# Kernel optimization log

Measured on AMD Instinct MI355X. Metric: run time of the kernel, lower is better.

The kernel has to match this reference:

```python
import jax, jax.numpy as jnp
import numpy as np

N = 100_000      # nodes
E = 1_600_000    # edges
F_IN = 128       # node_features
H1, H2 = 50, 20  # GCLSTM hidden sizes (fixed in the model)


def _norm_weights(src, dst, w, n):
    # PyG get_laplacian(sym): remove self loops, deg over row, sym-normalize.
    w = jnp.where(src == dst, jnp.zeros_like(w), w)  # remove self-loops (weight 0)
    deg = jax.ops.segment_sum(w, src, num_segments=n)
    deg_safe = jnp.where(deg > 0, deg, jnp.ones_like(deg))
    dis = jnp.where(deg > 0, deg_safe ** -0.5, jnp.zeros_like(deg))
    return dis[src] * w * dis[dst]


def _lhat_matvec(x, src, dst, wn, n):
    # L_hat = 2*L/lambda_max - I with sym norm and lambda_max=2  =>  -D^-1/2 A D^-1/2
    return -jax.ops.segment_sum(wn[:, None] * x[src], dst, num_segments=n)


def _gclstm_cell(x, src, dst, wn, n, Wx, bx, theta, bconv, out_ch):
    # One GCLSTM step with H = C = 0 (the model passes H=C=None).
    H = jnp.zeros((n, out_ch), x.dtype)
    C = jnp.zeros((n, out_ch), x.dtype)
    # ChebConv(H) for all 4 gates: Tx_0 = H, Tx_1 = L_hat @ H   (K = 2)
    Tx = jnp.stack([H, _lhat_matvec(H, src, dst, wn, n)])       # [2, n, out]
    conv = jnp.einsum('knf,gkfo->gno', Tx, theta) + bconv[:, None, :]  # [4, n, out]
    Z = x @ Wx + bx                                              # [n, 4*out], gates i,f,c,o
    zi, zf, zc, zo = jnp.split(Z, 4, axis=-1)
    I = jax.nn.sigmoid(zi + conv[0])
    Fg = jax.nn.sigmoid(zf + conv[1])
    T = jnp.tanh(zc + conv[2])
    C = Fg * C + I * T
    O = jax.nn.sigmoid(zo + conv[3])
    return O * jnp.tanh(C)


def setup_inputs() -> dict:
    key = jax.random.key(0)
    ks = jax.random.split(key, 14)
    s = 0.1  # param init scale
    return {
        'x': jax.random.normal(ks[0], (N, F_IN), jnp.float32),
        'edge_index': jax.random.randint(ks[1], (2, E), 0, N, dtype=jnp.int32),
        'edge_weight': jax.random.uniform(ks[2], (E,), jnp.float32),
        # layer 1: W_x for gates i,f,c,o concatenated, Cheb thetas [gate, K, in, out]
        'Wx1': s * jax.random.normal(ks[3], (F_IN, 4 * H1), jnp.float32),
        'bx1': s * jax.random.normal(ks[4], (4 * H1,), jnp.float32),
        'theta1': s * jax.random.normal(ks[5], (4, 2, H1, H1), jnp.float32),
        'bconv1': s * jax.random.normal(ks[6], (4, H1), jnp.float32),
        # layer 2
        'Wx2': s * jax.random.normal(ks[7], (H1, 4 * H2), jnp.float32),
        'bx2': s * jax.random.normal(ks[8], (4 * H2,), jnp.float32),
        'theta2': s * jax.random.normal(ks[9], (4, 2, H2, H2), jnp.float32),
        'bconv2': s * jax.random.normal(ks[10], (4, H2), jnp.float32),
        # linear head
        'Wl': s * jax.random.normal(ks[11], (H2, 1), jnp.float32),
        'bl': s * jax.random.normal(ks[12], (1,), jnp.float32),
    }


def reference(x, edge_index, edge_weight, Wx1, bx1, theta1, bconv1,
              Wx2, bx2, theta2, bconv2, Wl, bl):
    src, dst = edge_index[0], edge_index[1]
    wn = _norm_weights(src, dst, edge_weight, N)
    h = _gclstm_cell(x, src, dst, wn, N, Wx1, bx1, theta1, bconv1, H1)
    h = _gclstm_cell(h, src, dst, wn, N, Wx2, bx2, theta2, bconv2, H2)
    h = jax.nn.relu(h)
    # F.dropout: identity at inference (deterministic baseline)
    return h @ Wl + bl  # [N, 1]
```

## Files before the change

kernel.cpp:

```cpp
#include <hip/hip_runtime.h>


#define NODES 100000
#define NTILES 6250

typedef float v4f   __attribute__((ext_vector_type(4)));
typedef float fragC __attribute__((ext_vector_type(4)));
typedef short frag8 __attribute__((ext_vector_type(8)));

#define OFF_B1H 0
#define OFF_B2H 40960
#define OFF_B2L 49152
#define OFF_BIAS1 57344
#define OFF_BIAS2 57984
#define OFF_WL 58240
#define OFF_BL 58320

__device__ __forceinline__ unsigned short f2bf(float f) {
  unsigned int u = __float_as_uint(f);
  u += 0x7fffu + ((u >> 16) & 1u);
  return (unsigned short)(u >> 16);
}
__device__ __forceinline__ float bf2f(unsigned short h) {
  return __uint_as_float(((unsigned int)h) << 16);
}
__device__ __forceinline__ float fsig(float z) {
  float t = __builtin_amdgcn_exp2f(z * -1.44269504088896f);
  return __builtin_amdgcn_rcpf(1.0f + t);
}
__device__ __forceinline__ float ftanh(float z) {
  float t = __builtin_amdgcn_exp2f(z * 2.88539008177793f);
  return 1.0f - 2.0f * __builtin_amdgcn_rcpf(t + 1.0f);
}

__device__ __forceinline__ void cvt8(const float* v, frag8& hi, frag8& lo) {
#pragma unroll
  for (int j = 0; j < 8; ++j) {
    unsigned short hs = f2bf(v[j]);
    float fh = bf2f(hs);
    hi[j] = (short)hs;
    lo[j] = (short)f2bf(v[j] - fh);
  }
}

__global__ void pack_weights(const float* __restrict__ Wx1, const float* __restrict__ bx1,
                             const float* __restrict__ bconv1,
                             const float* __restrict__ Wx2, const float* __restrict__ bx2,
                             const float* __restrict__ bconv2,
                             const float* __restrict__ Wl, const float* __restrict__ bl,
                             unsigned char* __restrict__ ws) {
  const int tid = blockIdx.x * blockDim.x + threadIdx.x;
  const int stride = gridDim.x * blockDim.x;
  unsigned short* B1H = (unsigned short*)(ws + OFF_B1H);
  unsigned short* B2H = (unsigned short*)(ws + OFF_B2H);
  unsigned short* B2L = (unsigned short*)(ws + OFF_B2L);
  float* BIAS1 = (float*)(ws + OFF_BIAS1);
  float* BIAS2 = (float*)(ws + OFF_BIAS2);
  float* WLp = (float*)(ws + OFF_WL);
  float* BLp = (float*)(ws + OFF_BL);

  for (int idx = tid; idx < 20480; idx += stride) {
    int j = idx & 7, lane = (idx >> 3) & 63, ft = idx >> 9;
    int s = ft / 10, t = ft % 10;
    int k = 32 * s + ((lane >> 4) << 3) + j;
    int n = 16 * t + (lane & 15);
    float val = 0.f;
    if (n < 150) {
      int g = n / 50, ch = n % 50;
      int gs = (g == 0) ? 0 : (g == 1) ? 2 : 3;
      val = Wx1[k * 200 + gs * 50 + ch];
    }
    B1H[idx] = f2bf(val);
  }
  for (int idx = tid; idx < 4096; idx += stride) {
    int j = idx & 7, lane = (idx >> 3) & 63, ft = idx >> 9;
    int s = ft >> 2, t = ft & 3;
    int k = 32 * s + ((lane >> 4) << 3) + j;
    int n = 16 * t + (lane & 15);
    float val = 0.f;
    if (k < 50 && n < 60) {
      int g = n / 20, ch = n % 20;
      int gs = (g == 0) ? 0 : (g == 1) ? 2 : 3;
      val = Wx2[k * 80 + gs * 20 + ch];
    }
    unsigned short h = f2bf(val);
    B2H[idx] = h;
    B2L[idx] = f2bf(val - bf2f(h));
  }
  for (int idx = tid; idx < 160; idx += stride) {
    float v = 0.f;
    if (idx < 150) {
      int g = idx / 50, ch = idx % 50;
      int gs = (g == 0) ? 0 : (g == 1) ? 2 : 3;
      v = bx1[gs * 50 + ch] + bconv1[gs * 50 + ch];
    }
    BIAS1[idx] = v;
  }
  for (int idx = tid; idx < 64; idx += stride) {
    float v = 0.f;
    if (idx < 60) {
      int g = idx / 20, ch = idx % 20;
      int gs = (g == 0) ? 0 : (g == 1) ? 2 : 3;
      v = bx2[gs * 20 + ch] + bconv2[gs * 20 + ch];
    }
    BIAS2[idx] = v;
  }
  for (int idx = tid; idx < 20; idx += stride) WLp[idx] = Wl[idx];
  if (tid == 0) BLp[0] = bl[0];
}

__global__ __launch_bounds__(256, 1) void gclstm_main(
    const float* __restrict__ x, const unsigned char* __restrict__ wsb,
    float* __restrict__ out) {
  __shared__ float sZ[4][16 * 161];
  __shared__ float sH[4][16 * 76];
  __shared__ float sBias1[160];
  __shared__ float sBias2[64];
  __shared__ float sWl[20];

  const int tid = threadIdx.x;
  const int lane = tid & 63;
  const int wave = tid >> 6;
  const int m = lane & 15;
  const int q = lane >> 4;

  if (tid < 160) sBias1[tid] = ((const float*)(wsb + OFF_BIAS1))[tid];
  if (tid < 64) sBias2[tid] = ((const float*)(wsb + OFF_BIAS2))[tid];
  if (tid < 20) sWl[tid] = ((const float*)(wsb + OFF_WL))[tid];
  for (int i = tid; i < 4 * 16 * 76; i += 256) ((float*)sH)[i] = 0.f;
  const float blv = *(const float*)(wsb + OFF_BL);
  __syncthreads();

  frag8 b1h[40], b2h[8], b2l[8];
  {
    const frag8* g1 = (const frag8*)(wsb + OFF_B1H);
#pragma unroll
    for (int i = 0; i < 40; ++i) b1h[i] = g1[i * 64 + lane];
    const frag8* g2h = (const frag8*)(wsb + OFF_B2H);
    const frag8* g2l = (const frag8*)(wsb + OFF_B2L);
#pragma unroll
    for (int i = 0; i < 8; ++i) {
      b2h[i] = g2h[i * 64 + lane];
      b2l[i] = g2l[i * 64 + lane];
    }
  }

  float* sZw = (float*)sZ + wave * (16 * 161);
  float* sHw = (float*)sH + wave * (16 * 76);
  const int gw = blockIdx.x * 4 + wave;

  v4f abuf[8];
  int tau = gw;
  {
    const float* xr = x + (size_t)(tau * 16 + m) * 128 + q * 8;
#pragma unroll
    for (int s = 0; s < 4; ++s) {
      abuf[2 * s] = *(const v4f*)(xr + 32 * s);
      abuf[2 * s + 1] = *(const v4f*)(xr + 32 * s + 4);
    }
  }

  for (; tau < NTILES; tau += 1024) {
    frag8 ah[4], al[4];
#pragma unroll
    for (int s = 0; s < 4; ++s) {
      float av[8];
      *(v4f*)(av) = abuf[2 * s];
      *(v4f*)(av + 4) = abuf[2 * s + 1];
      cvt8(av, ah[s], al[s]);
    }
    int tn = tau + 1024;
    if (tn < NTILES) {
      const float* xr = x + (size_t)(tn * 16 + m) * 128 + q * 8;
#pragma unroll
      for (int s = 0; s < 4; ++s) {
        abuf[2 * s] = *(const v4f*)(xr + 32 * s);
        abuf[2 * s + 1] = *(const v4f*)(xr + 32 * s + 4);
      }
    }

    fragC acc[10];
#pragma unroll
    for (int t = 0; t < 10; ++t) acc[t] = (fragC){0.f, 0.f, 0.f, 0.f};
#pragma unroll
    for (int s = 0; s < 4; ++s) {
#pragma unroll
      for (int t = 0; t < 10; ++t) {
        acc[t] = __builtin_amdgcn_mfma_f32_16x16x32_bf16(ah[s], b1h[s * 10 + t], acc[t], 0, 0, 0);
        acc[t] = __builtin_amdgcn_mfma_f32_16x16x32_bf16(al[s], b1h[s * 10 + t], acc[t], 0, 0, 0);
      }
    }
#pragma unroll
    for (int t = 0; t < 10; ++t)
#pragma unroll
      for (int r = 0; r < 4; ++r)
        sZw[(q * 4 + r) * 161 + t * 16 + m] = acc[t][r];

#pragma unroll
    for (int it = 0; it < 13; ++it) {
      int jj = q + 4 * it;
      if (jj < 50) {
        float zi = sZw[m * 161 + jj] + sBias1[jj];
        float zc = sZw[m * 161 + 50 + jj] + sBias1[50 + jj];
        float zo = sZw[m * 161 + 100 + jj] + sBias1[100 + jj];
        float I = fsig(zi), T = ftanh(zc), O = fsig(zo);
        sHw[m * 76 + jj] = O * ftanh(I * T);
      }
    }

    frag8 hh[2], hl[2];
#pragma unroll
    for (int s = 0; s < 2; ++s) {
      float hv[8];
      *(v4f*)(hv) = *(const v4f*)(sHw + m * 76 + 32 * s + q * 8);
      *(v4f*)(hv + 4) = *(const v4f*)(sHw + m * 76 + 32 * s + q * 8 + 4);
      cvt8(hv, hh[s], hl[s]);
    }
    fragC acc2[4];
#pragma unroll
    for (int t = 0; t < 4; ++t) acc2[t] = (fragC){0.f, 0.f, 0.f, 0.f};
#pragma unroll
    for (int s = 0; s < 2; ++s)
#pragma unroll
      for (int t = 0; t < 4; ++t) {
        acc2[t] = __builtin_amdgcn_mfma_f32_16x16x32_bf16(hh[s], b2h[s * 4 + t], acc2[t], 0, 0, 0);
        acc2[t] = __builtin_amdgcn_mfma_f32_16x16x32_bf16(hl[s], b2h[s * 4 + t], acc2[t], 0, 0, 0);
        acc2[t] = __builtin_amdgcn_mfma_f32_16x16x32_bf16(hh[s], b2l[s * 4 + t], acc2[t], 0, 0, 0);
      }
#pragma unroll
    for (int t = 0; t < 4; ++t)
#pragma unroll
      for (int r = 0; r < 4; ++r)
        sZw[(q * 4 + r) * 161 + t * 16 + m] = acc2[t][r];

    float part = 0.f;
#pragma unroll
    for (int it = 0; it < 5; ++it) {
      int jj = q + 4 * it;
      float zi = sZw[m * 161 + jj] + sBias2[jj];
      float zc = sZw[m * 161 + 20 + jj] + sBias2[20 + jj];
      float zo = sZw[m * 161 + 40 + jj] + sBias2[40 + jj];
      float I = fsig(zi), T = ftanh(zc), O = fsig(zo);
      float h2 = O * ftanh(I * T);
      part += fmaxf(h2, 0.f) * sWl[jj];
    }
    part += __shfl_xor(part, 16);
    part += __shfl_xor(part, 32);
    if (q == 0) out[tau * 16 + m] = part + blv;
  }
}

extern "C" void kernel_launch(void* const* d_in, const int* in_sizes, int n_in,
                              void* d_out, int out_size, void* d_ws, size_t ws_size,
                              hipStream_t stream) {
  (void)in_sizes; (void)n_in; (void)out_size; (void)ws_size;
  const float* x = (const float*)d_in[0];
  const float* Wx1 = (const float*)d_in[3];
  const float* bx1 = (const float*)d_in[4];
  const float* bconv1 = (const float*)d_in[6];
  const float* Wx2 = (const float*)d_in[7];
  const float* bx2 = (const float*)d_in[8];
  const float* bconv2 = (const float*)d_in[10];
  const float* Wl = (const float*)d_in[11];
  const float* bl = (const float*)d_in[12];
  unsigned char* ws = (unsigned char*)d_ws;

  hipLaunchKernelGGL(pack_weights, dim3(32), dim3(256), 0, stream,
                     Wx1, bx1, bconv1, Wx2, bx2, bconv2, Wl, bl, ws);
  hipLaunchKernelGGL(gclstm_main, dim3(256), dim3(256), 0, stream,
                     x, ws, (float*)d_out);
}
```

Measured before the change: 138.6 us.

## Move layer-1 weights to LDS, interleave gate columns, double occupancy

Layer-1 B fragments move from 40 register-held frag8s into a shared LDS copy. Weight columns are re-packed so the i/c/o gates of each channel land in matching MFMA tiles, letting the gate activations be computed directly from accumulators instead of through an LDS round-trip. Biases are folded into the accumulator initialisation, the hi/lo bf16 split uses the paired conversion intrinsic, and the grid doubles to 512 blocks with launch bounds allowing 2 blocks per CU. This trades register pressure and LDS staging traffic for per-MFMA LDS reads of the weights, aiming to hide the memory latency of streaming x.

```diff
diff --git a/kernel.cpp b/kernel.cpp
--- a/kernel.cpp
+++ b/kernel.cpp
@@ -1,8 +1,11 @@
 #include <hip/hip_runtime.h>
+#include <hip/hip_bf16.h>
 
 
 #define NODES 100000
 #define NTILES 6250
+#define GRID_BLOCKS 512
+#define WAVES_TOTAL 2048
 
 typedef float v4f   __attribute__((ext_vector_type(4)));
 typedef float fragC __attribute__((ext_vector_type(4)));
@@ -11,10 +14,8 @@
 #define OFF_B1H 0
 #define OFF_B2H 40960
 #define OFF_B2L 49152
-#define OFF_BIAS1 57344
-#define OFF_BIAS2 57984
-#define OFF_WL 58240
-#define OFF_BL 58320
+#define OFF_PB1 57344
+#define OFF_PB2 57984
 
 __device__ __forceinline__ unsigned short f2bf(float f) {
   unsigned int u = __float_as_uint(f);
@@ -33,13 +34,23 @@
   return 1.0f - 2.0f * __builtin_amdgcn_rcpf(t + 1.0f);
 }
 
+union bfu { __hip_bfloat162 h; unsigned int u; };
+
 __device__ __forceinline__ void cvt8(const float* v, frag8& hi, frag8& lo) {
-#pragma unroll
-  for (int j = 0; j < 8; ++j) {
-    unsigned short hs = f2bf(v[j]);
-    float fh = bf2f(hs);
-    hi[j] = (short)hs;
-    lo[j] = (short)f2bf(v[j] - fh);
+  float lof[8];
+#pragma unroll
+  for (int p = 0; p < 4; ++p) {
+    bfu c; c.h = __float22bfloat162_rn(make_float2(v[2 * p], v[2 * p + 1]));
+    hi[2 * p]     = (short)(c.u & 0xffffu);
+    hi[2 * p + 1] = (short)(c.u >> 16);
+    lof[2 * p]     = v[2 * p]     - __uint_as_float((c.u & 0xffffu) << 16);
+    lof[2 * p + 1] = v[2 * p + 1] - __uint_as_float(c.u & 0xffff0000u);
+  }
+#pragma unroll
+  for (int p = 0; p < 4; ++p) {
+    bfu c; c.h = __float22bfloat162_rn(make_float2(lof[2 * p], lof[2 * p + 1]));
+    lo[2 * p]     = (short)(c.u & 0xffffu);
+    lo[2 * p + 1] = (short)(c.u >> 16);
   }
 }
 
@@ -47,28 +58,27 @@
                              const float* __restrict__ bconv1,
                              const float* __restrict__ Wx2, const float* __restrict__ bx2,
                              const float* __restrict__ bconv2,
-                             const float* __restrict__ Wl, const float* __restrict__ bl,
                              unsigned char* __restrict__ ws) {
   const int tid = blockIdx.x * blockDim.x + threadIdx.x;
   const int stride = gridDim.x * blockDim.x;
   unsigned short* B1H = (unsigned short*)(ws + OFF_B1H);
   unsigned short* B2H = (unsigned short*)(ws + OFF_B2H);
   unsigned short* B2L = (unsigned short*)(ws + OFF_B2L);
-  float* BIAS1 = (float*)(ws + OFF_BIAS1);
-  float* BIAS2 = (float*)(ws + OFF_BIAS2);
-  float* WLp = (float*)(ws + OFF_WL);
-  float* BLp = (float*)(ws + OFF_BL);
+  float* PB1 = (float*)(ws + OFF_PB1);
+  float* PB2 = (float*)(ws + OFF_PB2);
 
   for (int idx = tid; idx < 20480; idx += stride) {
     int j = idx & 7, lane = (idx >> 3) & 63, ft = idx >> 9;
     int s = ft / 10, t = ft % 10;
     int k = 32 * s + ((lane >> 4) << 3) + j;
-    int n = 16 * t + (lane & 15);
+    int m = lane & 15;
+    int c = -1, g = 0;
+    if (t <= 8) { g = t % 3; c = 16 * (t / 3) + m; }
+    else if (m < 6) { c = 48 + m / 3; g = m % 3; }
     float val = 0.f;
-    if (n < 150) {
-      int g = n / 50, ch = n % 50;
+    if (c >= 0) {
       int gs = (g == 0) ? 0 : (g == 1) ? 2 : 3;
-      val = Wx1[k * 200 + gs * 50 + ch];
+      val = Wx1[k * 200 + gs * 50 + c];
     }
     B1H[idx] = f2bf(val);
   }
@@ -79,44 +89,44 @@
     int n = 16 * t + (lane & 15);
     float val = 0.f;
     if (k < 50 && n < 60) {
-      int g = n / 20, ch = n % 20;
+      int g = n / 20, cc = n % 20;
       int gs = (g == 0) ? 0 : (g == 1) ? 2 : 3;
-      val = Wx2[k * 80 + gs * 20 + ch];
+      val = Wx2[k * 80 + gs * 20 + cc];
     }
     unsigned short h = f2bf(val);
     B2H[idx] = h;
     B2L[idx] = f2bf(val - bf2f(h));
   }
   for (int idx = tid; idx < 160; idx += stride) {
+    int t = idx >> 4, m = idx & 15;
+    int c = -1, g = 0;
+    if (t <= 8) { g = t % 3; c = 16 * (t / 3) + m; }
+    else if (m < 6) { c = 48 + m / 3; g = m % 3; }
     float v = 0.f;
-    if (idx < 150) {
-      int g = idx / 50, ch = idx % 50;
+    if (c >= 0) {
       int gs = (g == 0) ? 0 : (g == 1) ? 2 : 3;
-      v = bx1[gs * 50 + ch] + bconv1[gs * 50 + ch];
-    }
-    BIAS1[idx] = v;
+      v = bx1[gs * 50 + c] + bconv1[gs * 50 + c];
+    }
+    PB1[idx] = v;
   }
   for (int idx = tid; idx < 64; idx += stride) {
     float v = 0.f;
     if (idx < 60) {
-      int g = idx / 20, ch = idx % 20;
+      int g = idx / 20, cc = idx % 20;
       int gs = (g == 0) ? 0 : (g == 1) ? 2 : 3;
-      v = bx2[gs * 20 + ch] + bconv2[gs * 20 + ch];
-    }
-    BIAS2[idx] = v;
-  }
-  for (int idx = tid; idx < 20; idx += stride) WLp[idx] = Wl[idx];
-  if (tid == 0) BLp[0] = bl[0];
-}
-
-__global__ __launch_bounds__(256, 1) void gclstm_main(
+      v = bx2[gs * 20 + cc] + bconv2[gs * 20 + cc];
+    }
+    PB2[idx] = v;
+  }
+}
+
+__global__ __launch_bounds__(256, 2) void gclstm_main(
     const float* __restrict__ x, const unsigned char* __restrict__ wsb,
+    const float* __restrict__ Wl, const float* __restrict__ bl,
     float* __restrict__ out) {
-  __shared__ float sZ[4][16 * 161];
-  __shared__ float sH[4][16 * 76];
-  __shared__ float sBias1[160];
-  __shared__ float sBias2[64];
-  __shared__ float sWl[20];
+  __shared__ short sB1[20480];
+  __shared__ float sH[4][16 * 68];
+  __shared__ float sT9[4][16 * 6];
 
   const int tid = threadIdx.x;
   const int lane = tid & 63;
@@ -124,18 +134,15 @@
   const int m = lane & 15;
   const int q = lane >> 4;
 
-  if (tid < 160) sBias1[tid] = ((const float*)(wsb + OFF_BIAS1))[tid];
-  if (tid < 64) sBias2[tid] = ((const float*)(wsb + OFF_BIAS2))[tid];
-  if (tid < 20) sWl[tid] = ((const float*)(wsb + OFF_WL))[tid];
-  for (int i = tid; i < 4 * 16 * 76; i += 256) ((float*)sH)[i] = 0.f;
-  const float blv = *(const float*)(wsb + OFF_BL);
+  {
+    const v4f* g = (const v4f*)(wsb + OFF_B1H);
+    v4f* s = (v4f*)sB1;
+    for (int i = tid; i < 2560; i += 256) s[i] = g[i];
+  }
   __syncthreads();
 
-  frag8 b1h[40], b2h[8], b2l[8];
+  frag8 b2h[8], b2l[8];
   {
-    const frag8* g1 = (const frag8*)(wsb + OFF_B1H);
-#pragma unroll
-    for (int i = 0; i < 40; ++i) b1h[i] = g1[i * 64 + lane];
     const frag8* g2h = (const frag8*)(wsb + OFF_B2H);
     const frag8* g2l = (const frag8*)(wsb + OFF_B2L);
 #pragma unroll
@@ -144,14 +151,27 @@
       b2l[i] = g2l[i * 64 + lane];
     }
   }
-
-  float* sZw = (float*)sZ + wave * (16 * 161);
-  float* sHw = (float*)sH + wave * (16 * 76);
+  float bias1v[10], bias2v[4], wlv[5];
+  {
+    const float* pb1 = (const float*)(wsb + OFF_PB1);
+    const float* pb2 = (const float*)(wsb + OFF_PB2);
+#pragma unroll
+    for (int t = 0; t < 10; ++t) bias1v[t] = pb1[16 * t + m];
+#pragma unroll
+    for (int t = 0; t < 4; ++t) bias2v[t] = pb2[16 * t + m];
+#pragma unroll
+    for (int it = 0; it < 5; ++it) wlv[it] = Wl[q + 4 * it];
+  }
+  const float blv = bl[0];
+
+  float* sHw = (float*)sH + wave * (16 * 68);
+  float* sT9w = (float*)sT9 + wave * (16 * 6);
+  const frag8* sB1f = (const frag8*)sB1;
   const int gw = blockIdx.x * 4 + wave;
 
   v4f abuf[8];
   int tau = gw;
-  {
+  if (tau < NTILES) {
     const float* xr = x + (size_t)(tau * 16 + m) * 128 + q * 8;
 #pragma unroll
     for (int s = 0; s < 4; ++s) {
@@ -160,16 +180,16 @@
     }
   }
 
-  for (; tau < NTILES; tau += 1024) {
+  for (; tau < NTILES; tau += WAVES_TOTAL) {
     frag8 ah[4], al[4];
 #pragma unroll
     for (int s = 0; s < 4; ++s) {
       float av[8];
-      *(v4f*)(av) = abuf[2 * s];
+      *(v4f*)av = abuf[2 * s];
       *(v4f*)(av + 4) = abuf[2 * s + 1];
       cvt8(av, ah[s], al[s]);
     }
-    int tn = tau + 1024;
+    int tn = tau + WAVES_TOTAL;
     if (tn < NTILES) {
       const float* xr = x + (size_t)(tn * 16 + m) * 128 + q * 8;
 #pragma unroll
@@ -181,44 +201,54 @@
 
     fragC acc[10];
 #pragma unroll
-    for (int t = 0; t < 10; ++t) acc[t] = (fragC){0.f, 0.f, 0.f, 0.f};
-#pragma unroll
-    for (int s = 0; s < 4; ++s) {
+    for (int t = 0; t < 10; ++t)
+      acc[t] = (fragC){bias1v[t], bias1v[t], bias1v[t], bias1v[t]};
+#pragma unroll
+    for (int s = 0; s < 4; ++s)
 #pragma unroll
       for (int t = 0; t < 10; ++t) {
-        acc[t] = __builtin_amdgcn_mfma_f32_16x16x32_bf16(ah[s], b1h[s * 10 + t], acc[t], 0, 0, 0);
-        acc[t] = __builtin_amdgcn_mfma_f32_16x16x32_bf16(al[s], b1h[s * 10 + t], acc[t], 0, 0, 0);
+        frag8 b = sB1f[(s * 10 + t) * 64 + lane];
+        acc[t] = __builtin_amdgcn_mfma_f32_16x16x32_bf16(ah[s], b, acc[t], 0, 0, 0);
+        acc[t] = __builtin_amdgcn_mfma_f32_16x16x32_bf16(al[s], b, acc[t], 0, 0, 0);
       }
-    }
-#pragma unroll
-    for (int t = 0; t < 10; ++t)
-#pragma unroll
-      for (int r = 0; r < 4; ++r)
-        sZw[(q * 4 + r) * 161 + t * 16 + m] = acc[t][r];
-
-#pragma unroll
-    for (int it = 0; it < 13; ++it) {
-      int jj = q + 4 * it;
-      if (jj < 50) {
-        float zi = sZw[m * 161 + jj] + sBias1[jj];
-        float zc = sZw[m * 161 + 50 + jj] + sBias1[50 + jj];
-        float zo = sZw[m * 161 + 100 + jj] + sBias1[100 + jj];
-        float I = fsig(zi), T = ftanh(zc), O = fsig(zo);
-        sHw[m * 76 + jj] = O * ftanh(I * T);
+
+#pragma unroll
+    for (int b = 0; b < 3; ++b)
+#pragma unroll
+      for (int r = 0; r < 4; ++r) {
+        float I = fsig(acc[3 * b][r]);
+        float T = ftanh(acc[3 * b + 1][r]);
+        float O = fsig(acc[3 * b + 2][r]);
+        sHw[(q * 4 + r) * 68 + 16 * b + m] = O * ftanh(I * T);
       }
+    if (m >= 2) {
+#pragma unroll
+      for (int r = 0; r < 4; ++r) sHw[(q * 4 + r) * 68 + 48 + m] = 0.f;
+    }
+    if (m < 6) {
+#pragma unroll
+      for (int r = 0; r < 4; ++r) sT9w[(q * 4 + r) * 6 + m] = acc[9][r];
+    }
+    if (lane < 32) {
+      int row = lane & 15, cc = lane >> 4;
+      float I = fsig(sT9w[row * 6 + 3 * cc]);
+      float T = ftanh(sT9w[row * 6 + 3 * cc + 1]);
+      float O = fsig(sT9w[row * 6 + 3 * cc + 2]);
+      sHw[row * 68 + 48 + cc] = O * ftanh(I * T);
     }
 
     frag8 hh[2], hl[2];
 #pragma unroll
     for (int s = 0; s < 2; ++s) {
       float hv[8];
-      *(v4f*)(hv) = *(const v4f*)(sHw + m * 76 + 32 * s + q * 8);
-      *(v4f*)(hv + 4) = *(const v4f*)(sHw + m * 76 + 32 * s + q * 8 + 4);
+      *(v4f*)hv = *(const v4f*)(sHw + m * 68 + 32 * s + q * 8);
+      *(v4f*)(hv + 4) = *(const v4f*)(sHw + m * 68 + 32 * s + q * 8 + 4);
       cvt8(hv, hh[s], hl[s]);
     }
     fragC acc2[4];
 #pragma unroll
-    for (int t = 0; t < 4; ++t) acc2[t] = (fragC){0.f, 0.f, 0.f, 0.f};
+    for (int t = 0; t < 4; ++t)
+      acc2[t] = (fragC){bias2v[t], bias2v[t], bias2v[t], bias2v[t]};
 #pragma unroll
     for (int s = 0; s < 2; ++s)
 #pragma unroll
@@ -231,18 +261,17 @@
     for (int t = 0; t < 4; ++t)
 #pragma unroll
       for (int r = 0; r < 4; ++r)
-        sZw[(q * 4 + r) * 161 + t * 16 + m] = acc2[t][r];
+        sHw[(q * 4 + r) * 68 + 16 * t + m] = acc2[t][r];
 
     float part = 0.f;
 #pragma unroll
     for (int it = 0; it < 5; ++it) {
       int jj = q + 4 * it;
-      float zi = sZw[m * 161 + jj] + sBias2[jj];
-      float zc = sZw[m * 161 + 20 + jj] + sBias2[20 + jj];
-      float zo = sZw[m * 161 + 40 + jj] + sBias2[40 + jj];
-      float I = fsig(zi), T = ftanh(zc), O = fsig(zo);
+      float I = fsig(sHw[m * 68 + jj]);
+      float T = ftanh(sHw[m * 68 + 20 + jj]);
+      float O = fsig(sHw[m * 68 + 40 + jj]);
       float h2 = O * ftanh(I * T);
-      part += fmaxf(h2, 0.f) * sWl[jj];
+      part += fmaxf(h2, 0.f) * wlv[it];
     }
     part += __shfl_xor(part, 16);
     part += __shfl_xor(part, 32);
@@ -266,7 +295,7 @@
   unsigned char* ws = (unsigned char*)d_ws;
 
   hipLaunchKernelGGL(pack_weights, dim3(32), dim3(256), 0, stream,
-                     Wx1, bx1, bconv1, Wx2, bx2, bconv2, Wl, bl, ws);
-  hipLaunchKernelGGL(gclstm_main, dim3(256), dim3(256), 0, stream,
-                     x, ws, (float*)d_out);
-}
+                     Wx1, bx1, bconv1, Wx2, bx2, bconv2, ws);
+  hipLaunchKernelGGL(gclstm_main, dim3(GRID_BLOCKS), dim3(256), 0, stream,
+                     x, ws, Wl, bl, (float*)d_out);
+}
```

After: 206.9 us. +49.2%, slower.
